# Kernel tuning notes

Measured on AMD Instinct MI355X. Metric: run time of the kernel, lower is better.

The kernel has to match this reference:

```python
import jax, jax.numpy as jnp
import numpy as np

D_H = 1024

def _binary_operator(e_i, e_j):
    a_i, kv_i = e_i
    a_j, kv_j = e_j
    return (a_j * a_i, a_j * kv_i + kv_j)

def setup_inputs() -> dict:
    key = jax.random.key(0)
    k1, k2 = jax.random.split(key)
    B, S, D = 4, 4096, 1024
    x = jax.random.normal(k1, (B, S, D), dtype=jnp.float32)
    # nn.Dense default lecun_normal-ish scale; plain scaled normal is fine for a reference
    W = jax.random.normal(k2, (D, 3 * D_H), dtype=jnp.float32) * (1.0 / np.sqrt(D))
    b = jnp.zeros((3 * D_H,), dtype=jnp.float32)
    return {"x": x, "W": W, "b": b}

def reference(x, W, b):
    # projection: (B,S,D) @ (D, 3*d_h)
    proj = jnp.einsum('bsd,dh->bsh', x, W) + b
    inp = jnp.tanh(proj[:, :, :D_H])                 # (B,S,d_h)
    gates = jax.nn.sigmoid(proj[:, :, D_H:])         # (B,S,2*d_h)
    input_gate, output_gate = jnp.split(gates, 2, axis=-1)
    forget_gate = 1.0 - input_gate                   # tied gates
    _, hidden = jax.lax.associative_scan(
        _binary_operator, (forget_gate, inp * input_gate), axis=1)
    return jnp.tanh(hidden) * output_gate            # (B,S,d_h)
```

## Files before the change

### kernel.cpp

```cpp
#include <hip/hip_runtime.h>
#include <hip/hip_bf16.h>
#include <cmath>

typedef _Float16 half8 __attribute__((ext_vector_type(8)));
typedef _Float16 half4 __attribute__((ext_vector_type(4)));
typedef float f32x4 __attribute__((ext_vector_type(4)));

#define M_DIM 16384
#define K_DIM 1024
#define N_DIM 3072
#define S_LEN 4096
#define NCHUNK 64
#define CLEN 64

#define BUF_E 32768
#define B_OFF 16384

__device__ __forceinline__ float sigmoid_f(float x) {
    return 1.0f / (1.0f + __expf(-x));
}

__global__ void k_cast_x(const float* __restrict__ x, _Float16* __restrict__ xb) {
    int i = blockIdx.x * blockDim.x + threadIdx.x;
    float4 v = reinterpret_cast<const float4*>(x)[i];
    half4 h;
    h.x = (_Float16)v.x; h.y = (_Float16)v.y;
    h.z = (_Float16)v.z; h.w = (_Float16)v.w;
    reinterpret_cast<half4*>(xb)[i] = h;
}

__global__ void k_cast_w(const float* __restrict__ W, _Float16* __restrict__ Wt) {
    __shared__ float t[64][65];
    const int k0 = (blockIdx.x / 48) * 64;
    const int n0 = (blockIdx.x % 48) * 64;
    const int c  = threadIdx.x & 63;
    const int r0 = threadIdx.x >> 6;
    #pragma unroll
    for (int i = 0; i < 16; ++i) {
        int r = r0 + i * 4;
        t[r][c] = W[(size_t)(k0 + r) * N_DIM + n0 + c];
    }
    __syncthreads();
    #pragma unroll
    for (int i = 0; i < 16; ++i) {
        int r = r0 + i * 4;
        Wt[(size_t)(n0 + r) * K_DIM + k0 + c] = (_Float16)t[c][r];
    }
}

__global__ __launch_bounds__(512, 2) void k_gemm(
    const _Float16* __restrict__ A,
    const _Float16* __restrict__ Bt,
    const float* __restrict__ bias,
    _Float16* __restrict__ G)
{
    extern __shared__ _Float16 lds[];

    const int tid  = threadIdx.x;
    const int lane = tid & 63;
    const int wid  = tid >> 6;
    const int wr   = wid >> 2;
    const int wc   = wid & 3;

    const int bid   = blockIdx.x;
    const int wg    = (bid & 7) * 96 + (bid >> 3);
    const int tileM = (wg / 12) * 256;
    const int tileN = (wg % 12) * 256;

    const int l3   = lane >> 3;
    const int c8   = lane & 7;
    const int scol = ((c8 ^ l3) << 3);
    const _Float16* gA = A  + (size_t)(tileM + wid * 8 + l3) * K_DIM + scol;
    const _Float16* gB = Bt + (size_t)(tileN + wid * 8 + l3) * K_DIM + scol;
    _Float16* const sA = lds + wid * 512;
    _Float16* const sB = lds + B_OFF + wid * 512;

    const int l15 = lane & 15;
    const int hi  = lane >> 4;
    const int swz = (l15 & 7) << 3;
    const int o0  = (hi * 8)      ^ swz;
    const int o1  = (32 + hi * 8) ^ swz;
    const _Float16* arow = lds + (wr * 128 + l15) * 64;
    const _Float16* brow = lds + B_OFF + (wc * 64 + l15) * 64;

    f32x4 acc[8][4] = {};
    half8 a[4][2], b[4][2];

#define GL(SRC, DST) __builtin_amdgcn_global_load_lds( \
        (const __attribute__((address_space(1))) void*)(SRC), \
        (__attribute__((address_space(3))) void*)(DST), 16, 0, 0)

#define STAGE_A(kt, half, bufe) do { \
        const _Float16* g_ = gA + (size_t)(kt) * 64 + (size_t)((half) * 128) * K_DIM; \
        GL(g_,                       sA + (bufe) + (half) * 8192);        \
        GL(g_ + (size_t)64 * K_DIM,  sA + (bufe) + (half) * 8192 + 4096); \
    } while (0)

#define STAGE_B(kt, half, bufe) do { \
        const _Float16* g_ = gB + (size_t)(kt) * 64 + (size_t)((half) * 128) * K_DIM; \
        GL(g_,                       sB + (bufe) + (half) * 8192);        \
        GL(g_ + (size_t)64 * K_DIM,  sB + (bufe) + (half) * 8192 + 4096); \
    } while (0)

#define RD_A(bufe, mh) do { const _Float16* p_ = arow + (bufe) + (mh) * 4096; \
        a[0][0] = *(const half8*)(p_ + o0);        a[0][1] = *(const half8*)(p_ + o1); \
        a[1][0] = *(const half8*)(p_ + 1024 + o0); a[1][1] = *(const half8*)(p_ + 1024 + o1); \
        a[2][0] = *(const half8*)(p_ + 2048 + o0); a[2][1] = *(const half8*)(p_ + 2048 + o1); \
        a[3][0] = *(const half8*)(p_ + 3072 + o0); a[3][1] = *(const half8*)(p_ + 3072 + o1); \
    } while (0)

#define RD_B(bufe, nh) do { const _Float16* p_ = brow + (bufe) + (nh) * 2048; \
        b[(nh)*2+0][0] = *(const half8*)(p_ + o0);        b[(nh)*2+0][1] = *(const half8*)(p_ + o1); \
        b[(nh)*2+1][0] = *(const half8*)(p_ + 1024 + o0); b[(nh)*2+1][1] = *(const half8*)(p_ + 1024 + o1); \
    } while (0)

#define MFMA_Q(mh, nh) do { \
        __builtin_amdgcn_s_setprio(1); \
        _Pragma("unroll") \
        for (int m_ = 0; m_ < 4; ++m_) { \
            _Pragma("unroll") \
            for (int n_ = 0; n_ < 2; ++n_) { \
                acc[(mh)*4+m_][(nh)*2+n_] = __builtin_amdgcn_mfma_f32_16x16x32_f16( \
                    a[m_][0], b[(nh)*2+n_][0], acc[(mh)*4+m_][(nh)*2+n_], 0, 0, 0); \
                acc[(mh)*4+m_][(nh)*2+n_] = __builtin_amdgcn_mfma_f32_16x16x32_f16( \
                    a[m_][1], b[(nh)*2+n_][1], acc[(mh)*4+m_][(nh)*2+n_], 0, 0, 0); \
            } } \
        __builtin_amdgcn_s_setprio(0); \
    } while (0)

#define BAR() do { __builtin_amdgcn_s_barrier(); asm volatile("" ::: "memory"); } while (0)
#define VM4() asm volatile("s_waitcnt vmcnt(4)" ::: "memory")
#define VM0() asm volatile("s_waitcnt vmcnt(0)" ::: "memory")

    STAGE_B(0, 0, 0); STAGE_B(0, 1, 0);
    STAGE_A(0, 0, 0); STAGE_A(0, 1, 0);
    STAGE_B(1, 0, BUF_E); STAGE_A(1, 0, BUF_E);
    VM4();
    BAR();

    #pragma unroll 1
    for (int it = 0; it < 8; ++it) {
        const int kt0 = 2 * it;
        RD_A(0, 0); RD_B(0, 0);
        STAGE_B(kt0 + 1, 1, BUF_E);
        BAR(); MFMA_Q(0, 0); BAR();
        RD_B(0, 1);
        STAGE_A(kt0 + 1, 1, BUF_E);
        BAR(); MFMA_Q(0, 1); BAR();
        RD_A(0, 1);
        if (it < 7) STAGE_B(kt0 + 2, 0, 0);
        BAR(); MFMA_Q(1, 0); BAR();
        if (it < 7) { STAGE_B(kt0 + 2, 1, 0); VM4(); } else { VM0(); }
        BAR(); MFMA_Q(1, 1); BAR();
        RD_A(BUF_E, 0); RD_B(BUF_E, 0);
        if (it < 7) STAGE_A(kt0 + 2, 0, 0);
        BAR(); MFMA_Q(0, 0); BAR();
        RD_B(BUF_E, 1);
        if (it < 7) STAGE_A(kt0 + 2, 1, 0);
        BAR(); MFMA_Q(0, 1); BAR();
        RD_A(BUF_E, 1);
        if (it < 7) STAGE_B(kt0 + 3, 0, BUF_E);
        BAR(); MFMA_Q(1, 0); BAR();
        if (it < 7) { STAGE_A(kt0 + 3, 0, BUF_E); VM4(); }
        BAR(); MFMA_Q(1, 1); BAR();
    }

#undef STAGE_A
#undef STAGE_B
#undef RD_A
#undef RD_B
#undef MFMA_Q
#undef GL

    #pragma unroll
    for (int j = 0; j < 4; ++j) {
        const int n = tileN + wc * 64 + j * 16 + l15;
        const float bn = bias[n];
        const bool is_tanh = (n < 1024);
        #pragma unroll
        for (int i = 0; i < 8; ++i) {
            const int mb = tileM + wr * 128 + i * 16 + hi * 4;
            #pragma unroll
            for (int r = 0; r < 4; ++r) {
                float v = acc[i][j][r] + bn;
                G[(size_t)(mb + r) * N_DIM + n] = (_Float16)(is_tanh ? tanhf(v) : sigmoid_f(v));
            }
        }
    }
}

__global__ void k_scan1(const _Float16* __restrict__ G,
                        float* __restrict__ sumA, float* __restrict__ sumH) {
    const int gid   = blockIdx.x;
    const int dblk  = gid & 3;
    const int chunk = (gid >> 2) & 63;
    const int b     = gid >> 8;
    const int d     = dblk * 256 + threadIdx.x;

    const _Float16* base = G + (size_t)(b * S_LEN + chunk * CLEN) * N_DIM;
    float A = 1.0f, H = 0.0f;
    #pragma unroll 4
    for (int s = 0; s < CLEN; ++s) {
        float g0 = (float)base[(size_t)s * N_DIM + d];
        float g1 = (float)base[(size_t)s * N_DIM + 1024 + d];
        float a  = 1.0f - g1;
        float kv = g0 * g1;
        H = fmaf(a, H, kv);
        A *= a;
    }
    const int cidx = (b * NCHUNK + chunk) * 1024 + d;
    sumA[cidx] = A;
    sumH[cidx] = H;
}

__global__ void k_scan2(const float* __restrict__ sumA, const float* __restrict__ sumH,
                        float* __restrict__ pref) {
    const int c = blockIdx.x * blockDim.x + threadIdx.x;
    const int b = c >> 10;
    const int d = c & 1023;
    float h = 0.0f;
    #pragma unroll 8
    for (int chunk = 0; chunk < NCHUNK; ++chunk) {
        const int idx = (b * NCHUNK + chunk) * 1024 + d;
        pref[idx] = h;
        h = fmaf(sumA[idx], h, sumH[idx]);
    }
}

__global__ void k_scan3(const _Float16* __restrict__ G,
                        const float* __restrict__ pref,
                        float* __restrict__ out) {
    const int gid   = blockIdx.x;
    const int dblk  = gid & 3;
    const int chunk = (gid >> 2) & 63;
    const int b     = gid >> 8;
    const int d     = dblk * 256 + threadIdx.x;

    const _Float16* base = G + (size_t)(b * S_LEN + chunk * CLEN) * N_DIM;
    float h = pref[(b * NCHUNK + chunk) * 1024 + d];
    #pragma unroll 4
    for (int s = 0; s < CLEN; ++s) {
        float g0 = (float)base[(size_t)s * N_DIM + d];
        float g1 = (float)base[(size_t)s * N_DIM + 1024 + d];
        float g2 = (float)base[(size_t)s * N_DIM + 2048 + d];
        float a  = 1.0f - g1;
        float kv = g0 * g1;
        h = fmaf(a, h, kv);
        out[(size_t)(b * S_LEN + chunk * CLEN + s) * 1024 + d] = tanhf(h) * g2;
    }
}

extern "C" void kernel_launch(void* const* d_in, const int* in_sizes, int n_in,
                              void* d_out, int out_size, void* d_ws, size_t ws_size,
                              hipStream_t stream) {
    const float* x = (const float*)d_in[0];
    const float* W = (const float*)d_in[1];
    const float* b = (const float*)d_in[2];
    float* out = (float*)d_out;

    char* ws = (char*)d_ws;
    _Float16* xb = (_Float16*)ws;
    _Float16* Wt = (_Float16*)(ws + 33554432);
    _Float16* G  = (_Float16*)(ws + 33554432 + 6291456);
    float* sumA  = (float*)(ws + 140509184);
    float* sumH  = sumA + 4096 * NCHUNK;
    float* pref  = sumH + 4096 * NCHUNK;

    k_cast_x<<<16384, 256, 0, stream>>>(x, xb);
    k_cast_w<<<768,   256, 0, stream>>>(W, Wt);
    k_gemm <<<768, 512, 131072, stream>>>(xb, Wt, b, G);
    k_scan1<<<1024, 256, 0, stream>>>(G, sumA, sumH);
    k_scan2<<<16,   256, 0, stream>>>(sumA, sumH, pref);
    k_scan3<<<1024, 256, 0, stream>>>(G, pref, out);
    (void)in_sizes; (void)n_in; (void)out_size; (void)ws_size;
}
```

Baseline: 219.4 us.

## Use fast transcendentals, retune GEMM phase barriers, vectorize scan kernels

```diff
diff --git a/kernel.cpp b/kernel.cpp
--- a/kernel.cpp
+++ b/kernel.cpp
@@ -16,8 +16,13 @@
 #define BUF_E 32768
 #define B_OFF 16384
 
-__device__ __forceinline__ float sigmoid_f(float x) {
-    return 1.0f / (1.0f + __expf(-x));
+__device__ __forceinline__ float fast_sigmoid(float x) {
+    return __builtin_amdgcn_rcpf(1.0f + __expf(-x));
+}
+__device__ __forceinline__ float fast_tanh(float x) {
+    float t = __expf(-2.0f * __builtin_fabsf(x));
+    float y = (1.0f - t) * __builtin_amdgcn_rcpf(1.0f + t);
+    return __builtin_copysignf(y, x);
 }
 
 __global__ void k_cast_x(const float* __restrict__ x, _Float16* __restrict__ xb) {
@@ -118,51 +123,62 @@
         __builtin_amdgcn_s_setprio(1); \
         _Pragma("unroll") \
         for (int m_ = 0; m_ < 4; ++m_) { \
-            _Pragma("unroll") \
-            for (int n_ = 0; n_ < 2; ++n_) { \
-                acc[(mh)*4+m_][(nh)*2+n_] = __builtin_amdgcn_mfma_f32_16x16x32_f16( \
-                    a[m_][0], b[(nh)*2+n_][0], acc[(mh)*4+m_][(nh)*2+n_], 0, 0, 0); \
-                acc[(mh)*4+m_][(nh)*2+n_] = __builtin_amdgcn_mfma_f32_16x16x32_f16( \
-                    a[m_][1], b[(nh)*2+n_][1], acc[(mh)*4+m_][(nh)*2+n_], 0, 0, 0); \
-            } } \
+            acc[(mh)*4+m_][(nh)*2+0] = __builtin_amdgcn_mfma_f32_16x16x32_f16( \
+                a[m_][0], b[(nh)*2+0][0], acc[(mh)*4+m_][(nh)*2+0], 0, 0, 0); \
+            acc[(mh)*4+m_][(nh)*2+1] = __builtin_amdgcn_mfma_f32_16x16x32_f16( \
+                a[m_][0], b[(nh)*2+1][0], acc[(mh)*4+m_][(nh)*2+1], 0, 0, 0); } \
+        _Pragma("unroll") \
+        for (int m_ = 0; m_ < 4; ++m_) { \
+            acc[(mh)*4+m_][(nh)*2+0] = __builtin_amdgcn_mfma_f32_16x16x32_f16( \
+                a[m_][1], b[(nh)*2+0][1], acc[(mh)*4+m_][(nh)*2+0], 0, 0, 0); \
+            acc[(mh)*4+m_][(nh)*2+1] = __builtin_amdgcn_mfma_f32_16x16x32_f16( \
+                a[m_][1], b[(nh)*2+1][1], acc[(mh)*4+m_][(nh)*2+1], 0, 0, 0); } \
         __builtin_amdgcn_s_setprio(0); \
     } while (0)
 
-#define BAR() do { __builtin_amdgcn_s_barrier(); asm volatile("" ::: "memory"); } while (0)
-#define VM4() asm volatile("s_waitcnt vmcnt(4)" ::: "memory")
-#define VM0() asm volatile("s_waitcnt vmcnt(0)" ::: "memory")
+#define SCHED0() __builtin_amdgcn_sched_barrier(0)
+#define PHASE_MID() do { SCHED0(); __builtin_amdgcn_s_barrier(); \
+        asm volatile("s_waitcnt lgkmcnt(0)" ::: "memory"); SCHED0(); } while (0)
+#define PHASE_END() do { SCHED0(); __builtin_amdgcn_s_barrier(); \
+        asm volatile("" ::: "memory"); } while (0)
+#define LGKM8() asm volatile("s_waitcnt lgkmcnt(8)" ::: "memory")
+#define VM4()   asm volatile("s_waitcnt vmcnt(4)" ::: "memory")
+#define VM0()   asm volatile("s_waitcnt vmcnt(0)" ::: "memory")
 
     STAGE_B(0, 0, 0); STAGE_B(0, 1, 0);
     STAGE_A(0, 0, 0); STAGE_A(0, 1, 0);
     STAGE_B(1, 0, BUF_E); STAGE_A(1, 0, BUF_E);
     VM4();
-    BAR();
+    __builtin_amdgcn_s_barrier();
+    asm volatile("" ::: "memory");
 
     #pragma unroll 1
     for (int it = 0; it < 8; ++it) {
         const int kt0 = 2 * it;
         RD_A(0, 0); RD_B(0, 0);
         STAGE_B(kt0 + 1, 1, BUF_E);
-        BAR(); MFMA_Q(0, 0); BAR();
+        LGKM8();
+        PHASE_MID(); MFMA_Q(0, 0); PHASE_END();
         RD_B(0, 1);
         STAGE_A(kt0 + 1, 1, BUF_E);
-        BAR(); MFMA_Q(0, 1); BAR();
+        PHASE_MID(); MFMA_Q(0, 1); PHASE_END();
         RD_A(0, 1);
         if (it < 7) STAGE_B(kt0 + 2, 0, 0);
-        BAR(); MFMA_Q(1, 0); BAR();
+        PHASE_MID(); MFMA_Q(1, 0); PHASE_END();
         if (it < 7) { STAGE_B(kt0 + 2, 1, 0); VM4(); } else { VM0(); }
-        BAR(); MFMA_Q(1, 1); BAR();
+        PHASE_MID(); MFMA_Q(1, 1); PHASE_END();
         RD_A(BUF_E, 0); RD_B(BUF_E, 0);
         if (it < 7) STAGE_A(kt0 + 2, 0, 0);
-        BAR(); MFMA_Q(0, 0); BAR();
+        LGKM8();
+        PHASE_MID(); MFMA_Q(0, 0); PHASE_END();
         RD_B(BUF_E, 1);
         if (it < 7) STAGE_A(kt0 + 2, 1, 0);
-        BAR(); MFMA_Q(0, 1); BAR();
+        PHASE_MID(); MFMA_Q(0, 1); PHASE_END();
         RD_A(BUF_E, 1);
         if (it < 7) STAGE_B(kt0 + 3, 0, BUF_E);
-        BAR(); MFMA_Q(1, 0); BAR();
+        PHASE_MID(); MFMA_Q(1, 0); PHASE_END();
         if (it < 7) { STAGE_A(kt0 + 3, 0, BUF_E); VM4(); }
-        BAR(); MFMA_Q(1, 1); BAR();
+        PHASE_MID(); MFMA_Q(1, 1); PHASE_END();
     }
 
 #undef STAGE_A
@@ -183,7 +199,8 @@
             #pragma unroll
             for (int r = 0; r < 4; ++r) {
                 float v = acc[i][j][r] + bn;
-                G[(size_t)(mb + r) * N_DIM + n] = (_Float16)(is_tanh ? tanhf(v) : sigmoid_f(v));
+                G[(size_t)(mb + r) * N_DIM + n] =
+                    (_Float16)(is_tanh ? fast_tanh(v) : fast_sigmoid(v));
             }
         }
     }
@@ -191,26 +208,29 @@
 
 __global__ void k_scan1(const _Float16* __restrict__ G,
                         float* __restrict__ sumA, float* __restrict__ sumH) {
-    const int gid   = blockIdx.x;
-    const int dblk  = gid & 3;
-    const int chunk = (gid >> 2) & 63;
-    const int b     = gid >> 8;
-    const int d     = dblk * 256 + threadIdx.x;
+    const int chunk = blockIdx.x & 63;
+    const int b     = blockIdx.x >> 6;
+    const int d0    = threadIdx.x * 4;
 
     const _Float16* base = G + (size_t)(b * S_LEN + chunk * CLEN) * N_DIM;
-    float A = 1.0f, H = 0.0f;
+    float A[4], H[4];
+    #pragma unroll
+    for (int j = 0; j < 4; ++j) { A[j] = 1.0f; H[j] = 0.0f; }
     #pragma unroll 4
     for (int s = 0; s < CLEN; ++s) {
-        float g0 = (float)base[(size_t)s * N_DIM + d];
-        float g1 = (float)base[(size_t)s * N_DIM + 1024 + d];
-        float a  = 1.0f - g1;
-        float kv = g0 * g1;
-        H = fmaf(a, H, kv);
-        A *= a;
-    }
-    const int cidx = (b * NCHUNK + chunk) * 1024 + d;
-    sumA[cidx] = A;
-    sumH[cidx] = H;
+        half4 v0 = *(const half4*)(base + (size_t)s * N_DIM + d0);
+        half4 v1 = *(const half4*)(base + (size_t)s * N_DIM + 1024 + d0);
+        #pragma unroll
+        for (int j = 0; j < 4; ++j) {
+            float g1 = (float)v1[j];
+            float a  = 1.0f - g1;
+            H[j] = fmaf(a, H[j], (float)v0[j] * g1);
+            A[j] *= a;
+        }
+    }
+    const int cidx = (b * NCHUNK + chunk) * 1024 + d0;
+    *(float4*)(sumA + cidx) = make_float4(A[0], A[1], A[2], A[3]);
+    *(float4*)(sumH + cidx) = make_float4(H[0], H[1], H[2], H[3]);
 }
 
 __global__ void k_scan2(const float* __restrict__ sumA, const float* __restrict__ sumH,
@@ -230,23 +250,31 @@
 __global__ void k_scan3(const _Float16* __restrict__ G,
                         const float* __restrict__ pref,
                         float* __restrict__ out) {
-    const int gid   = blockIdx.x;
-    const int dblk  = gid & 3;
-    const int chunk = (gid >> 2) & 63;
-    const int b     = gid >> 8;
-    const int d     = dblk * 256 + threadIdx.x;
+    const int chunk = blockIdx.x & 63;
+    const int b     = blockIdx.x >> 6;
+    const int d0    = threadIdx.x * 4;
 
     const _Float16* base = G + (size_t)(b * S_LEN + chunk * CLEN) * N_DIM;
-    float h = pref[(b * NCHUNK + chunk) * 1024 + d];
-    #pragma unroll 4
+    const int cidx = (b * NCHUNK + chunk) * 1024 + d0;
+    float h[4];
+    #pragma unroll
+    for (int j = 0; j < 4; ++j) h[j] = pref[cidx + j];
+
+    #pragma unroll 2
     for (int s = 0; s < CLEN; ++s) {
-        float g0 = (float)base[(size_t)s * N_DIM + d];
-        float g1 = (float)base[(size_t)s * N_DIM + 1024 + d];
-        float g2 = (float)base[(size_t)s * N_DIM + 2048 + d];
-        float a  = 1.0f - g1;
-        float kv = g0 * g1;
-        h = fmaf(a, h, kv);
-        out[(size_t)(b * S_LEN + chunk * CLEN + s) * 1024 + d] = tanhf(h) * g2;
+        half4 v0 = *(const half4*)(base + (size_t)s * N_DIM + d0);
+        half4 v1 = *(const half4*)(base + (size_t)s * N_DIM + 1024 + d0);
+        half4 v2 = *(const half4*)(base + (size_t)s * N_DIM + 2048 + d0);
+        float4 o;
+        #pragma unroll
+        for (int j = 0; j < 4; ++j) {
+            float g1 = (float)v1[j];
+            float a  = 1.0f - g1;
+            h[j] = fmaf(a, h[j], (float)v0[j] * g1);
+            float t = fast_tanh(h[j]) * (float)v2[j];
+            ((float*)&o)[j] = t;
+        }
+        *(float4*)(out + (size_t)(b * S_LEN + chunk * CLEN + s) * 1024 + d0) = o;
     }
 }
 
@@ -269,8 +297,8 @@
     k_cast_x<<<16384, 256, 0, stream>>>(x, xb);
     k_cast_w<<<768,   256, 0, stream>>>(W, Wt);
     k_gemm <<<768, 512, 131072, stream>>>(xb, Wt, b, G);
-    k_scan1<<<1024, 256, 0, stream>>>(G, sumA, sumH);
-    k_scan2<<<16,   256, 0, stream>>>(sumA, sumH, pref);
-    k_scan3<<<1024, 256, 0, stream>>>(G, pref, out);
+    k_scan1<<<256, 256, 0, stream>>>(G, sumA, sumH);
+    k_scan2<<<16,  256, 0, stream>>>(sumA, sumH, pref);
+    k_scan3<<<256, 256, 0, stream>>>(G, pref, out);
     (void)in_sizes; (void)n_in; (void)out_size; (void)ws_size;
 }
```

Result: faster. 193.7 us (-11.7%).
